# Performance work log

Measured on AMD Instinct MI355X. Metric: run time of the kernel, lower is better.

The kernel has to match this reference:

```python
import jax, jax.numpy as jnp
import numpy as np
import math

B, N, D, S = 128, 2048, 512, 64  # batch, nodes, d_model, state_features


def setup_inputs() -> dict:
    key = jax.random.key(0)
    k1, k2, k3, k4, k5 = jax.random.split(key, 5)
    node_embeddings = jax.random.normal(k1, (B, N, D), dtype=jnp.float32)
    truck_state = jax.random.normal(k2, (B, S), dtype=jnp.float32)
    mask = jax.random.bernoulli(k3, 0.3, (B, N))  # True = masked-out node
    Wq = jax.random.normal(k4, (D, S), dtype=jnp.float32) * 0.05  # query_proj weight
    bq = jnp.zeros((D,), dtype=jnp.float32)
    Ws = jax.random.normal(k5, (D, D), dtype=jnp.float32) * 0.02  # scores_proj weight
    bs = jnp.zeros((D,), dtype=jnp.float32)
    return {"node_embeddings": node_embeddings, "truck_state": truck_state,
            "mask": mask, "Wq": Wq, "bq": bq, "Ws": Ws, "bs": bs}


def reference(node_embeddings, truck_state, mask, Wq, bq, Ws, bs):
    d_model = node_embeddings.shape[-1]
    scale = 1.0 / math.sqrt(d_model)
    # query = query_proj(truck_state): [B, D]
    query = truck_state @ Wq.T + bq
    # single-query attention scores over nodes: [B, N]
    attn_scores = jnp.einsum('bd,bnd->bn', query, node_embeddings) * scale
    attn_scores = jnp.where(mask, -jnp.inf, attn_scores)
    attn_weights = jax.nn.softmax(attn_scores, axis=-1)
    # context: [B, D]
    context = jnp.einsum('bn,bnd->bd', attn_weights, node_embeddings)
    # scores = scores_proj(context): [B, D]
    scores = context @ Ws.T + bs
    # dot-product logits per node: [B, N]
    logits = jnp.einsum('bnd,bd->bn', node_embeddings, scores) * scale
    logits = jnp.where(mask, -jnp.inf, logits)
    return logits
```

## Files before the change

### kernel.cpp

```cpp
#include <hip/hip_runtime.h>
#include <math.h>

#define BB 128
#define NN 2048
#define DD 512
#define SS 64
#define NCH 8
#define CH (NN / NCH)
#define NPW (CH / 8)
#define SCALE 0.044194173824159216f
#define NEG_BIG (-1.0e30f)

__device__ __forceinline__ float dot8(float4 a0, float4 a1, float4 b0, float4 b1) {
    return a0.x*b0.x + a0.y*b0.y + a0.z*b0.z + a0.w*b0.w
         + a1.x*b1.x + a1.y*b1.y + a1.z*b1.z + a1.w*b1.w;
}

__global__ __launch_bounds__(512, 8) void k_pass1(
    const float* __restrict__ node, const unsigned char* __restrict__ mask,
    const float* __restrict__ ts, const float* __restrict__ Wq,
    const float* __restrict__ bq,
    float* __restrict__ part_ctx, float* __restrict__ part_m,
    float* __restrict__ part_l)
{
    int bid   = blockIdx.x;
    int b     = bid >> 3;
    int chunk = bid & 7;
    int wave  = threadIdx.x >> 6;
    int lane  = threadIdx.x & 63;
    int dbase = lane * 8;

    __shared__ float q_lds[DD];
    __shared__ float lds_ctx[8][DD];
    __shared__ float lds_m[8], lds_l[8];

    {
        int d = threadIdx.x;
        const float4* tv = (const float4*)(ts + b * SS);
        const float4* wv = (const float4*)(Wq + (size_t)d * SS);
        float acc = 0.f;
#pragma unroll
        for (int k = 0; k < SS / 4; ++k) {
            float4 a = tv[k], w = wv[k];
            acc += a.x*w.x + a.y*w.y + a.z*w.z + a.w*w.w;
        }
        q_lds[d] = acc + bq[d];
    }

    int n0 = chunk * CH + wave * NPW;
    const unsigned char* mrow = mask + (size_t)b * NN;
    unsigned long long bal = __ballot(mrow[n0 + (lane & 31)] == 0);
    unsigned int live = (unsigned int)(bal & 0xffffffffull);
    __syncthreads();

    float4 q0 = *(const float4*)&q_lds[dbase];
    float4 q1 = *(const float4*)&q_lds[dbase + 4];

    float m = NEG_BIG, l = 0.f;
    float c0=0,c1=0,c2=0,c3=0,c4=0,c5=0,c6=0,c7=0;
    const float* rp = node + ((size_t)b * NN + n0) * DD + dbase;

#pragma unroll 1
    for (int j = 0; j < NPW; j += 2) {
        float4 v0a = *(const float4*)rp;
        float4 v0b = *(const float4*)(rp + 4);
        const float* rp1 = rp + DD;
        float4 v1a = *(const float4*)rp1;
        float4 v1b = *(const float4*)(rp1 + 4);
        rp += 2 * DD;
        float dp0 = dot8(q0, q1, v0a, v0b);
        float dp1 = dot8(q0, q1, v1a, v1b);
#pragma unroll
        for (int off = 32; off; off >>= 1) {
            dp0 += __shfl_xor(dp0, off, 64);
            dp1 += __shfl_xor(dp1, off, 64);
        }
        bool a0 = (live >> j) & 1u;
        bool a1 = (live >> (j + 1)) & 1u;
        float s0 = a0 ? dp0 * SCALE : NEG_BIG;
        float s1 = a1 ? dp1 * SCALE : NEG_BIG;
        float nm = fmaxf(m, fmaxf(s0, s1));
        float r  = __expf(m - nm);
        float p0 = a0 ? __expf(s0 - nm) : 0.f;
        float p1 = a1 ? __expf(s1 - nm) : 0.f;
        l = l * r + p0 + p1;
        c0 = c0*r + p0*v0a.x + p1*v1a.x;
        c1 = c1*r + p0*v0a.y + p1*v1a.y;
        c2 = c2*r + p0*v0a.z + p1*v1a.z;
        c3 = c3*r + p0*v0a.w + p1*v1a.w;
        c4 = c4*r + p0*v0b.x + p1*v1b.x;
        c5 = c5*r + p0*v0b.y + p1*v1b.y;
        c6 = c6*r + p0*v0b.z + p1*v1b.z;
        c7 = c7*r + p0*v0b.w + p1*v1b.w;
        m = nm;
    }

    if (lane == 0) { lds_m[wave] = m; lds_l[wave] = l; }
    __syncthreads();
    float M = lds_m[0];
#pragma unroll
    for (int w = 1; w < 8; ++w) M = fmaxf(M, lds_m[w]);
    float f = __expf(m - M);
    *(float4*)&lds_ctx[wave][dbase]     = make_float4(c0*f, c1*f, c2*f, c3*f);
    *(float4*)&lds_ctx[wave][dbase + 4] = make_float4(c4*f, c5*f, c6*f, c7*f);
    __syncthreads();
    {
        int d = threadIdx.x;
        float acc = 0.f;
#pragma unroll
        for (int w = 0; w < 8; ++w) acc += lds_ctx[w][d];
        part_ctx[(size_t)bid * DD + d] = acc;
    }
    if (threadIdx.x == 0) {
        float L = 0.f;
#pragma unroll
        for (int w = 0; w < 8; ++w) L += __expf(lds_m[w] - M) * lds_l[w];
        part_m[bid] = M;
        part_l[bid] = L;
    }
}

__global__ __launch_bounds__(512) void k_combine(
    const float* __restrict__ part_ctx, const float* __restrict__ part_m,
    const float* __restrict__ part_l,
    const float* __restrict__ Ws, const float* __restrict__ bs,
    float* __restrict__ scores)
{
    int b    = blockIdx.x;
    int wave = threadIdx.x >> 6;
    int lane = threadIdx.x & 63;
    int dbase = lane * 8;
    __shared__ float ctx[DD];

    float M = NEG_BIG;
#pragma unroll
    for (int c = 0; c < NCH; ++c) M = fmaxf(M, part_m[(b << 3) | c]);
    float fc[NCH];
    float L = 0.f;
#pragma unroll
    for (int c = 0; c < NCH; ++c) {
        fc[c] = __expf(part_m[(b << 3) | c] - M);
        L += fc[c] * part_l[(b << 3) | c];
    }
    float Linv = 1.f / fmaxf(L, 1e-30f);

    {
        int d = threadIdx.x;
        float acc = 0.f;
#pragma unroll
        for (int c = 0; c < NCH; ++c)
            acc += fc[c] * part_ctx[(size_t)((b << 3) | c) * DD + d];
        ctx[d] = acc * Linv;
    }
    __syncthreads();

    float4 x0 = *(const float4*)&ctx[dbase];
    float4 x1 = *(const float4*)&ctx[dbase + 4];
    for (int j = 0; j < 64; ++j) {
        int dd = wave * 64 + j;
        const float* wrow = Ws + (size_t)dd * DD + dbase;
        float4 w0 = *(const float4*)wrow;
        float4 w1 = *(const float4*)(wrow + 4);
        float dp = dot8(x0, x1, w0, w1);
#pragma unroll
        for (int off = 32; off; off >>= 1) dp += __shfl_xor(dp, off, 64);
        if (lane == 0) scores[b * DD + dd] = dp + bs[dd];
    }
}

__global__ __launch_bounds__(256, 8) void k_logits(
    const float* __restrict__ node, const unsigned char* __restrict__ mask,
    const float* __restrict__ scores, float* __restrict__ out)
{
    int wave = threadIdx.x >> 6;
    int lane = threadIdx.x & 63;
    int dbase = lane * 8;
    int wg = blockIdx.x * 4 + wave;
    int rg = 32767 - wg;
    int g0 = rg * 8;
    int b  = g0 >> 11;

    const float* sc = scores + b * DD + dbase;
    float4 t0 = *(const float4*)sc;
    float4 t1 = *(const float4*)(sc + 4);

#pragma unroll 1
    for (int i = 6; i >= 0; i -= 2) {
        int g1 = g0 + i + 1, g2 = g0 + i;
        const float* r1 = node + (size_t)g1 * DD + dbase;
        const float* r2 = node + (size_t)g2 * DD + dbase;
        float4 v1a = *(const float4*)r1, v1b = *(const float4*)(r1 + 4);
        float4 v2a = *(const float4*)r2, v2b = *(const float4*)(r2 + 4);
        unsigned char mk1 = mask[g1], mk2 = mask[g2];
        float dp1 = dot8(t0, t1, v1a, v1b);
        float dp2 = dot8(t0, t1, v2a, v2b);
#pragma unroll
        for (int off = 32; off; off >>= 1) {
            dp1 += __shfl_xor(dp1, off, 64);
            dp2 += __shfl_xor(dp2, off, 64);
        }
        if (lane == 0) {
            out[g1] = mk1 ? NEG_BIG : dp1 * SCALE;
            out[g2] = mk2 ? NEG_BIG : dp2 * SCALE;
        }
    }
}

extern "C" void kernel_launch(void* const* d_in, const int* in_sizes, int n_in,
                              void* d_out, int out_size, void* d_ws, size_t ws_size,
                              hipStream_t stream)
{
    const float*         node = (const float*)d_in[0];
    const float*         ts   = (const float*)d_in[1];
    const unsigned char* mask = (const unsigned char*)d_in[2];
    const float*         Wq   = (const float*)d_in[3];
    const float*         bq   = (const float*)d_in[4];
    const float*         Ws   = (const float*)d_in[5];
    const float*         bs   = (const float*)d_in[6];
    float* out = (float*)d_out;

    float* ws       = (float*)d_ws;
    float* part_ctx = ws;
    float* part_m   = part_ctx + BB * NCH * DD;
    float* part_l   = part_m + BB * NCH;
    float* scores   = part_l + BB * NCH;

    k_pass1  <<<BB * NCH, 512, 0, stream>>>(node, mask, ts, Wq, bq,
                                            part_ctx, part_m, part_l);
    k_combine<<<BB, 512, 0, stream>>>(part_ctx, part_m, part_l, Ws, bs, scores);
    k_logits <<<(BB * NN) / 32, 256, 0, stream>>>(node, mask, scores, out);
}
```

Before: 233.2 us.

## Split attention into more chunks, parallelize scores projection, skip masked rows in logits

Doubles the number of node chunks per batch in the first pass so more workgroups share the attention reduction. The combine kernel becomes four workgroups per batch, each computing a quarter of the output features. The logits kernel loads eight mask bytes at once and skips loading node rows for masked nodes. This spreads latency-bound work across more CUs and cuts memory reads for the roughly 30% of nodes that are masked, at the cost of more partial results to merge and some divergent control flow.

```diff
diff --git a/kernel.cpp b/kernel.cpp
--- a/kernel.cpp
+++ b/kernel.cpp
@@ -5,7 +5,7 @@
 #define NN 2048
 #define DD 512
 #define SS 64
-#define NCH 8
+#define NCH 16
 #define CH (NN / NCH)
 #define NPW (CH / 8)
 #define SCALE 0.044194173824159216f
@@ -24,8 +24,8 @@
     float* __restrict__ part_l)
 {
     int bid   = blockIdx.x;
-    int b     = bid >> 3;
-    int chunk = bid & 7;
+    int b     = bid >> 4;
+    int chunk = bid & 15;
     int wave  = threadIdx.x >> 6;
     int lane  = threadIdx.x & 63;
     int dbase = lane * 8;
@@ -49,8 +49,8 @@
 
     int n0 = chunk * CH + wave * NPW;
     const unsigned char* mrow = mask + (size_t)b * NN;
-    unsigned long long bal = __ballot(mrow[n0 + (lane & 31)] == 0);
-    unsigned int live = (unsigned int)(bal & 0xffffffffull);
+    unsigned long long bal = __ballot(mrow[n0 + (lane & 15)] == 0);
+    unsigned int live = (unsigned int)(bal & 0xffffull);
     __syncthreads();
 
     float4 q0 = *(const float4*)&q_lds[dbase];
@@ -120,13 +120,14 @@
     }
 }
 
-__global__ __launch_bounds__(512) void k_combine(
+__global__ __launch_bounds__(256) void k_scores(
     const float* __restrict__ part_ctx, const float* __restrict__ part_m,
     const float* __restrict__ part_l,
     const float* __restrict__ Ws, const float* __restrict__ bs,
     float* __restrict__ scores)
 {
-    int b    = blockIdx.x;
+    int b    = blockIdx.x >> 2;
+    int qt   = blockIdx.x & 3;
     int wave = threadIdx.x >> 6;
     int lane = threadIdx.x & 63;
     int dbase = lane * 8;
@@ -134,30 +135,29 @@
 
     float M = NEG_BIG;
 #pragma unroll
-    for (int c = 0; c < NCH; ++c) M = fmaxf(M, part_m[(b << 3) | c]);
+    for (int c = 0; c < NCH; ++c) M = fmaxf(M, part_m[(b << 4) | c]);
+    float L = 0.f;
     float fc[NCH];
-    float L = 0.f;
 #pragma unroll
     for (int c = 0; c < NCH; ++c) {
-        fc[c] = __expf(part_m[(b << 3) | c] - M);
-        L += fc[c] * part_l[(b << 3) | c];
+        fc[c] = __expf(part_m[(b << 4) | c] - M);
+        L += fc[c] * part_l[(b << 4) | c];
     }
     float Linv = 1.f / fmaxf(L, 1e-30f);
 
-    {
-        int d = threadIdx.x;
+    for (int d = threadIdx.x; d < DD; d += 256) {
         float acc = 0.f;
 #pragma unroll
         for (int c = 0; c < NCH; ++c)
-            acc += fc[c] * part_ctx[(size_t)((b << 3) | c) * DD + d];
+            acc += fc[c] * part_ctx[(size_t)((b << 4) | c) * DD + d];
         ctx[d] = acc * Linv;
     }
     __syncthreads();
 
     float4 x0 = *(const float4*)&ctx[dbase];
     float4 x1 = *(const float4*)&ctx[dbase + 4];
-    for (int j = 0; j < 64; ++j) {
-        int dd = wave * 64 + j;
+    for (int j = 0; j < 32; ++j) {
+        int dd = qt * 128 + wave * 32 + j;
         const float* wrow = Ws + (size_t)dd * DD + dbase;
         float4 w0 = *(const float4*)wrow;
         float4 w1 = *(const float4*)(wrow + 4);
@@ -180,29 +180,26 @@
     int g0 = rg * 8;
     int b  = g0 >> 11;
 
+    unsigned long long mb = *(const unsigned long long*)(mask + g0);
+
     const float* sc = scores + b * DD + dbase;
     float4 t0 = *(const float4*)sc;
     float4 t1 = *(const float4*)(sc + 4);
 
 #pragma unroll 1
-    for (int i = 6; i >= 0; i -= 2) {
-        int g1 = g0 + i + 1, g2 = g0 + i;
-        const float* r1 = node + (size_t)g1 * DD + dbase;
-        const float* r2 = node + (size_t)g2 * DD + dbase;
-        float4 v1a = *(const float4*)r1, v1b = *(const float4*)(r1 + 4);
-        float4 v2a = *(const float4*)r2, v2b = *(const float4*)(r2 + 4);
-        unsigned char mk1 = mask[g1], mk2 = mask[g2];
-        float dp1 = dot8(t0, t1, v1a, v1b);
-        float dp2 = dot8(t0, t1, v2a, v2b);
-#pragma unroll
-        for (int off = 32; off; off >>= 1) {
-            dp1 += __shfl_xor(dp1, off, 64);
-            dp2 += __shfl_xor(dp2, off, 64);
+    for (int i = 7; i >= 0; --i) {
+        int g = g0 + i;
+        if ((mb >> (8 * i)) & 0xffull) {
+            if (lane == 0) out[g] = NEG_BIG;
+            continue;
         }
-        if (lane == 0) {
-            out[g1] = mk1 ? NEG_BIG : dp1 * SCALE;
-            out[g2] = mk2 ? NEG_BIG : dp2 * SCALE;
-        }
+        const float* rp = node + (size_t)g * DD + dbase;
+        float4 va = *(const float4*)rp;
+        float4 vb = *(const float4*)(rp + 4);
+        float dp = dot8(t0, t1, va, vb);
+#pragma unroll
+        for (int off = 32; off; off >>= 1) dp += __shfl_xor(dp, off, 64);
+        if (lane == 0) out[g] = dp * SCALE;
     }
 }
 
@@ -225,8 +222,8 @@
     float* part_l   = part_m + BB * NCH;
     float* scores   = part_l + BB * NCH;
 
-    k_pass1  <<<BB * NCH, 512, 0, stream>>>(node, mask, ts, Wq, bq,
-                                            part_ctx, part_m, part_l);
-    k_combine<<<BB, 512, 0, stream>>>(part_ctx, part_m, part_l, Ws, bs, scores);
-    k_logits <<<(BB * NN) / 32, 256, 0, stream>>>(node, mask, scores, out);
-}
+    k_pass1 <<<BB * NCH, 512, 0, stream>>>(node, mask, ts, Wq, bq,
+                                           part_ctx, part_m, part_l);
+    k_scores<<<BB * 4, 256, 0, stream>>>(part_ctx, part_m, part_l, Ws, bs, scores);
+    k_logits<<<(BB * NN) / 32, 256, 0, stream>>>(node, mask, scores, out);
+}
```

Measured after the change: 209.5 us. 10.1% less time.
